# Kernel tuning notes

Hardware: AMD Instinct MI355X
Metric: run time of the kernel (lower is better)

Reference implementation:

```python
import jax, jax.numpy as jnp
import numpy as np

N = 200          # fixed by map_norm's .view(200, 1)
D = 8192         # in_features
EPS = 1e-5


def setup_inputs() -> dict:
    key = jax.random.key(0)
    ks = jax.random.split(key, 7)
    lim = float(np.sqrt(6.0 / D))
    x = jax.random.normal(ks[0], (N, D), dtype=jnp.float32)
    Wq = jax.random.uniform(ks[1], (D, D), dtype=jnp.float32, minval=-lim, maxval=lim)
    Wk = jax.random.uniform(ks[2], (D, D), dtype=jnp.float32, minval=-lim, maxval=lim)
    Wv = jax.random.uniform(ks[3], (D, D), dtype=jnp.float32, minval=-lim, maxval=lim)
    bq = jax.random.normal(ks[4], (D,), dtype=jnp.float32) * 0.01
    bk = jax.random.normal(ks[5], (D,), dtype=jnp.float32) * 0.01
    bv = jax.random.normal(ks[6], (D,), dtype=jnp.float32) * 0.01
    return {"x": x, "Wq": Wq, "bq": bq, "Wk": Wk, "bk": bk, "Wv": Wv, "bv": bv}


def reference(x, Wq, bq, Wk, bk, Wv, bv):
    d_out = x.shape[1]
    cc = jnp.sqrt(jnp.asarray(d_out, dtype=x.dtype))
    # nn.Linear: y = x @ W.T + b
    q = x @ Wq.T + bq          # [N, D]
    k = x @ Wk.T + bk          # [N, D]
    v = x @ Wv.T + bv          # [N, D]
    s = q @ k.T                # [N, N] score map
    mean = jnp.mean(s, axis=-1, keepdims=True)
    var = jnp.var(s, axis=-1, keepdims=True, ddof=1)  # torch.var is unbiased
    s = (s - mean) / jnp.sqrt(var + EPS)
    s = jnp.sin(s)
    scores = jax.nn.softmax(s / cc, axis=-1)
    return scores @ v          # [N, D]
```

## Files before the change

### kernel.cpp

```cpp
#include <hip/hip_runtime.h>
#include <hip/hip_bf16.h>
#include <cstdint>

#define DD 8192
#define NROW 200
#define MT 13
#define MPAD 208
#define KPV 256
#define EPSV 1e-5f
#define BK 64
#define ABUF_BYTES (MPAD * BK * 2)

using short8 = __attribute__((ext_vector_type(8))) short;
using f32x4  = __attribute__((ext_vector_type(4))) float;

#define MEMBAR asm volatile("" ::: "memory")

__device__ __forceinline__ ushort f2bf(float f) {
    union { float f; unsigned u; } c; c.f = f;
    unsigned u = c.u;
    return (ushort)((u + 0x7FFFu + ((u >> 16) & 1u)) >> 16);
}

__device__ __forceinline__ short8 pack8(float4 a, float4 b) {
    short8 o;
    o[0]=f2bf(a.x); o[1]=f2bf(a.y); o[2]=f2bf(a.z); o[3]=f2bf(a.w);
    o[4]=f2bf(b.x); o[5]=f2bf(b.y); o[6]=f2bf(b.z); o[7]=f2bf(b.w);
    return o;
}

__global__ void cvt_x(const float* __restrict__ x, ushort* __restrict__ xb) {
    int i = (blockIdx.x * 256 + threadIdx.x) * 8;
    int row = i >> 13;
    int col = i & (DD - 1);
    short8 o;
    if (row < NROW) {
        const float4* p = reinterpret_cast<const float4*>(x + (size_t)row * DD + col);
        float4 a = p[0], b = p[1];
        o = pack8(a, b);
    } else {
        for (int j = 0; j < 8; ++j) o[j] = 0;
    }
    *reinterpret_cast<short8*>(xb + i) = o;
}

__global__ __launch_bounds__(64) void qkv_gemm(
    const ushort* __restrict__ xb,
    const float* __restrict__ Wq, const float* __restrict__ Wk, const float* __restrict__ Wv,
    const float* __restrict__ bq, const float* __restrict__ bk, const float* __restrict__ bv,
    ushort* __restrict__ qb, ushort* __restrict__ kb, ushort* __restrict__ vt)
{
    __shared__ char Asm[2 * ABUF_BYTES];

    const int mat = blockIdx.y;
    const float* W    = (mat == 0) ? Wq : (mat == 1 ? Wk : Wv);
    const float* bias = (mat == 0) ? bq : (mat == 1 ? bk : bv);

    const int lane  = threadIdx.x;
    const int col16 = lane & 15;
    const int kgrp  = lane >> 4;
    const int ncol0 = blockIdx.x * 32 + col16;
    const int ncol1 = ncol0 + 16;

    const float* wp0 = W + (size_t)ncol0 * DD + kgrp * 8;
    const float* wp1 = W + (size_t)ncol1 * DD + kgrp * 8;

    const ushort* sbase = xb + (size_t)(lane >> 3) * DD
                             + (size_t)(((lane & 7) ^ ((lane >> 3) & 7)) * 8);

    const int b0off = col16 * 128 + ((kgrp ^ (col16 & 7)) * 16);
    const int b1off = b0off ^ 64;

    f32x4 acc0[MT], acc1[MT];
    #pragma unroll
    for (int m = 0; m < MT; ++m)
        for (int r = 0; r < 4; ++r) { acc0[m][r] = 0.f; acc1[m][r] = 0.f; }

#define STAGE(B, KK) { _Pragma("unroll") for (int r = 0; r < 26; ++r) { \
        __builtin_amdgcn_global_load_lds( \
            (const __attribute__((address_space(1))) void*)(sbase + (KK) + r * 8 * DD), \
            (__attribute__((address_space(3))) void*)(Asm + (B) * ABUF_BYTES + r * 1024), \
            16, 0, 0); } }

#define LOADW(d, KK) { \
        d##0 = *reinterpret_cast<const float4*>(wp0 + (KK)); \
        d##1 = *reinterpret_cast<const float4*>(wp0 + (KK) + 4); \
        d##2 = *reinterpret_cast<const float4*>(wp0 + (KK) + 32); \
        d##3 = *reinterpret_cast<const float4*>(wp0 + (KK) + 36); \
        d##4 = *reinterpret_cast<const float4*>(wp1 + (KK)); \
        d##5 = *reinterpret_cast<const float4*>(wp1 + (KK) + 4); \
        d##6 = *reinterpret_cast<const float4*>(wp1 + (KK) + 32); \
        d##7 = *reinterpret_cast<const float4*>(wp1 + (KK) + 36); }

#define COMPUTE(BASE, b00, b01, b10, b11) { \
        _Pragma("unroll") for (int m = 0; m < MT; ++m) { \
            short8 a0 = *reinterpret_cast<const short8*>(Asm + (BASE) + b0off + m * 2048); \
            acc0[m] = __builtin_amdgcn_mfma_f32_16x16x32_bf16(a0, b00, acc0[m], 0, 0, 0); \
            acc1[m] = __builtin_amdgcn_mfma_f32_16x16x32_bf16(a0, b10, acc1[m], 0, 0, 0); \
            short8 a1 = *reinterpret_cast<const short8*>(Asm + (BASE) + b1off + m * 2048); \
            acc0[m] = __builtin_amdgcn_mfma_f32_16x16x32_bf16(a1, b01, acc0[m], 0, 0, 0); \
            acc1[m] = __builtin_amdgcn_mfma_f32_16x16x32_bf16(a1, b11, acc1[m], 0, 0, 0); } }

    float4 wA0, wA1, wA2, wA3, wA4, wA5, wA6, wA7;
    float4 wB0, wB1, wB2, wB3, wB4, wB5, wB6, wB7;

    STAGE(0, 0);
    MEMBAR;
    LOADW(wA, 0);
    MEMBAR;
    LOADW(wB, BK);
    MEMBAR;

    for (int k0 = 0; k0 < DD; k0 += 2 * BK) {
        {
            short8 b00 = pack8(wA0, wA1);
            short8 b01 = pack8(wA2, wA3);
            short8 b10 = pack8(wA4, wA5);
            short8 b11 = pack8(wA6, wA7);
            STAGE(1, k0 + BK);
            MEMBAR;
            int kp = (k0 + 2 * BK) & (DD - 1);
            LOADW(wA, kp);
            MEMBAR;
            asm volatile("s_waitcnt vmcnt(42)" ::: "memory");
            COMPUTE(0, b00, b01, b10, b11);
        }
        {
            short8 b00 = pack8(wB0, wB1);
            short8 b01 = pack8(wB2, wB3);
            short8 b10 = pack8(wB4, wB5);
            short8 b11 = pack8(wB6, wB7);
            int kp1 = (k0 + 2 * BK) & (DD - 1);
            STAGE(0, kp1);
            MEMBAR;
            int kp2 = (k0 + 3 * BK) & (DD - 1);
            LOADW(wB, kp2);
            MEMBAR;
            asm volatile("s_waitcnt vmcnt(42)" ::: "memory");
            COMPUTE(ABUF_BYTES, b00, b01, b10, b11);
        }
    }
#undef STAGE
#undef LOADW
#undef COMPUTE

    const float badd0 = bias[ncol0];
    const float badd1 = bias[ncol1];
    if (mat < 2) {
        ushort* outb = (mat == 0) ? qb : kb;
        #pragma unroll
        for (int m = 0; m < MT; ++m)
            for (int r = 0; r < 4; ++r) {
                int row = m * 16 + kgrp * 4 + r;
                outb[(size_t)row * DD + ncol0] = f2bf(acc0[m][r] + badd0);
                outb[(size_t)row * DD + ncol1] = f2bf(acc1[m][r] + badd1);
            }
    } else {
        #pragma unroll
        for (int m = 0; m < MT; ++m)
            for (int r = 0; r < 4; ++r) {
                int row = m * 16 + kgrp * 4 + r;
                vt[(size_t)ncol0 * KPV + row] = f2bf(acc0[m][r] + badd0);
                vt[(size_t)ncol1 * KPV + row] = f2bf(acc1[m][r] + badd1);
            }
    }
}

__global__ __launch_bounds__(256) void sgemm(const ushort* __restrict__ qb, const ushort* __restrict__ kb,
                                             float* __restrict__ sbuf) {
    const int bm = blockIdx.y, bn = blockIdx.x;
    const int lane  = threadIdx.x & 63;
    const int wave  = threadIdx.x >> 6;
    const int col16 = lane & 15, kgrp = lane >> 4;
    const ushort* ap = qb + (size_t)(bm * 16 + col16) * DD + kgrp * 8;
    const ushort* bp = kb + (size_t)(bn * 16 + col16) * DD + kgrp * 8;
    f32x4 acc;
    for (int r = 0; r < 4; ++r) acc[r] = 0.f;
    const int kend = (wave + 1) * 2048;
    for (int k0 = wave * 2048; k0 < kend; k0 += 32) {
        short8 a = *reinterpret_cast<const short8*>(ap + k0);
        short8 b = *reinterpret_cast<const short8*>(bp + k0);
        acc = __builtin_amdgcn_mfma_f32_16x16x32_bf16(a, b, acc, 0, 0, 0);
    }
    __shared__ f32x4 red[4][64];
    red[wave][lane] = acc;
    __syncthreads();
    if (wave == 0) {
        f32x4 s = red[0][lane];
        for (int j = 1; j < 4; ++j) { f32x4 o = red[j][lane]; for (int r = 0; r < 4; ++r) s[r] += o[r]; }
        for (int r = 0; r < 4; ++r)
            sbuf[(size_t)(bm * 16 + kgrp * 4 + r) * MPAD + bn * 16 + col16] = s[r];
    }
}

__global__ __launch_bounds__(256) void rownorm(const float* __restrict__ sbuf, ushort* __restrict__ pb) {
    const int row = blockIdx.x;
    const int t = threadIdx.x;
    if (row >= NROW) { pb[(size_t)row * KPV + t] = 0; return; }
    __shared__ float part[4];
    const int lane = t & 63, wave = t >> 6;
    float x = (t < NROW) ? sbuf[(size_t)row * MPAD + t] : 0.f;

    float s = x;
    for (int m = 32; m; m >>= 1) s += __shfl_xor(s, m, 64);
    if (lane == 0) part[wave] = s;
    __syncthreads();
    float mean = (part[0] + part[1] + part[2] + part[3]) * (1.f / 200.f);

    float d = (t < NROW) ? (x - mean) : 0.f;
    float s2 = d * d;
    for (int m = 32; m; m >>= 1) s2 += __shfl_xor(s2, m, 64);
    __syncthreads();
    if (lane == 0) part[wave] = s2;
    __syncthreads();
    float var = (part[0] + part[1] + part[2] + part[3]) * (1.f / 199.f);

    float inv = 1.f / sqrtf(var + EPSV);
    float y = sinf(d * inv);
    const float inv_cc = 1.f / 90.50966799187809f;
    float e = (t < NROW) ? expf(y * inv_cc) : 0.f;

    float se = e;
    for (int m = 32; m; m >>= 1) se += __shfl_xor(se, m, 64);
    __syncthreads();
    if (lane == 0) part[wave] = se;
    __syncthreads();
    float tot = part[0] + part[1] + part[2] + part[3];
    pb[(size_t)row * KPV + t] = (t < NROW) ? f2bf(e / tot) : (ushort)0;
}

__global__ __launch_bounds__(256) void pv_gemm(const ushort* __restrict__ pb, const ushort* __restrict__ vt,
                                               float* __restrict__ out) {
    const int lane  = threadIdx.x & 63;
    const int wave  = threadIdx.x >> 6;
    const int col16 = lane & 15, kgrp = lane >> 4;
    const int ncol  = blockIdx.x * 64 + wave * 16 + col16;
    const ushort* ap = pb + (size_t)col16 * KPV + kgrp * 8;
    const ushort* bp = vt + (size_t)ncol  * KPV + kgrp * 8;
    f32x4 acc[MT];
    for (int m = 0; m < MT; ++m)
        for (int r = 0; r < 4; ++r) acc[m][r] = 0.f;
    for (int k0 = 0; k0 < KPV; k0 += 32) {
        short8 b = *reinterpret_cast<const short8*>(bp + k0);
        #pragma unroll
        for (int m = 0; m < MT; ++m) {
            short8 a = *reinterpret_cast<const short8*>(ap + (size_t)m * 16 * KPV + k0);
            acc[m] = __builtin_amdgcn_mfma_f32_16x16x32_bf16(a, b, acc[m], 0, 0, 0);
        }
    }
    for (int m = 0; m < MT; ++m)
        for (int r = 0; r < 4; ++r) {
            int row = m * 16 + kgrp * 4 + r;
            if (row < NROW) out[(size_t)row * DD + ncol] = acc[m][r];
        }
}

extern "C" void kernel_launch(void* const* d_in, const int* in_sizes, int n_in,
                              void* d_out, int out_size, void* d_ws, size_t ws_size,
                              hipStream_t stream) {
    const float* x  = (const float*)d_in[0];
    const float* Wq = (const float*)d_in[1];
    const float* bq = (const float*)d_in[2];
    const float* Wk = (const float*)d_in[3];
    const float* bk = (const float*)d_in[4];
    const float* Wv = (const float*)d_in[5];
    const float* bv = (const float*)d_in[6];
    float* out = (float*)d_out;

    char* ws = (char*)d_ws;
    ushort* xb   = (ushort*)(ws);
    ushort* qb   = (ushort*)(ws + 3407872);
    ushort* kb   = (ushort*)(ws + 6815744);
    ushort* vt   = (ushort*)(ws + 10223616);
    float*  sbuf = (float*)(ws + 14417920);
    ushort* pb   = (ushort*)(ws + 14590976);

    cvt_x<<<832, 256, 0, stream>>>(x, xb);
    qkv_gemm<<<dim3(256, 3), 64, 0, stream>>>(xb, Wq, Wk, Wv, bq, bk, bv, qb, kb, vt);
    sgemm<<<dim3(13, 13), 256, 0, stream>>>(qb, kb, sbuf);
    rownorm<<<208, 256, 0, stream>>>(sbuf, pb);
    pv_gemm<<<128, 256, 0, stream>>>(pb, vt, out);
}
```

Before: 284.2 us.

## Split QKV GEMM over K with 4-wave blocks sharing staged X tile

The QKV projection kernel now runs 256-thread blocks in which four waves share one LDS-staged X tile, each wave loading part of it. Blocks synchronise with barriers and the pipeline is a single double-buffered phase loop. When the workspace is large enough, K is split four ways. fp32 partial sums go to a workspace buffer and two new kernels reduce them, add the bias, convert to bf16 and transpose V. This aims to raise the number of waves per CU and improve latency hiding for the weight-bandwidth-bound GEMM, at the cost of extra partial-sum traffic, two extra launches and barrier overhead.

```diff
diff --git a/kernel.cpp b/kernel.cpp
--- a/kernel.cpp
+++ b/kernel.cpp
@@ -44,11 +44,12 @@
     *reinterpret_cast<short8*>(xb + i) = o;
 }
 
-__global__ __launch_bounds__(64) void qkv_gemm(
+__global__ __launch_bounds__(256, 3) void qkv_gemm(
     const ushort* __restrict__ xb,
     const float* __restrict__ Wq, const float* __restrict__ Wk, const float* __restrict__ Wv,
     const float* __restrict__ bq, const float* __restrict__ bk, const float* __restrict__ bv,
-    ushort* __restrict__ qb, ushort* __restrict__ kb, ushort* __restrict__ vt)
+    ushort* __restrict__ qb, ushort* __restrict__ kb, ushort* __restrict__ vt,
+    float* __restrict__ part, int kchunk)
 {
     __shared__ char Asm[2 * ABUF_BYTES];
 
@@ -56,17 +57,23 @@
     const float* W    = (mat == 0) ? Wq : (mat == 1 ? Wk : Wv);
     const float* bias = (mat == 0) ? bq : (mat == 1 ? bk : bv);
 
-    const int lane  = threadIdx.x;
+    const int t     = threadIdx.x;
+    const int lane  = t & 63;
+    const int wave  = t >> 6;
     const int col16 = lane & 15;
     const int kgrp  = lane >> 4;
-    const int ncol0 = blockIdx.x * 32 + col16;
+    const int ncol0 = blockIdx.x * 128 + wave * 32 + col16;
     const int ncol1 = ncol0 + 16;
+    const int kbase = blockIdx.z * kchunk;
+    const int kmask = kchunk - 1;
 
     const float* wp0 = W + (size_t)ncol0 * DD + kgrp * 8;
     const float* wp1 = W + (size_t)ncol1 * DD + kgrp * 8;
 
     const ushort* sbase = xb + (size_t)(lane >> 3) * DD
                              + (size_t)(((lane & 7) ^ ((lane >> 3) & 7)) * 8);
+    const int r0w = (wave < 2) ? wave * 7 : 14 + (wave - 2) * 6;
+    const int sw  = (wave < 2) ? 7 : 6;
 
     const int b0off = col16 * 128 + ((kgrp ^ (col16 & 7)) * 16);
     const int b1off = b0off ^ 64;
@@ -76,11 +83,11 @@
     for (int m = 0; m < MT; ++m)
         for (int r = 0; r < 4; ++r) { acc0[m][r] = 0.f; acc1[m][r] = 0.f; }
 
-#define STAGE(B, KK) { _Pragma("unroll") for (int r = 0; r < 26; ++r) { \
+#define STAGE(BOFF, KK) { _Pragma("unroll") for (int rr = 0; rr < 7; ++rr) { if (rr < sw) { \
         __builtin_amdgcn_global_load_lds( \
-            (const __attribute__((address_space(1))) void*)(sbase + (KK) + r * 8 * DD), \
-            (__attribute__((address_space(3))) void*)(Asm + (B) * ABUF_BYTES + r * 1024), \
-            16, 0, 0); } }
+            (const __attribute__((address_space(1))) void*)(sbase + (KK) + (size_t)(r0w + rr) * 8 * DD), \
+            (__attribute__((address_space(3))) void*)(Asm + (BOFF) + (r0w + rr) * 1024), \
+            16, 0, 0); } } }
 
 #define LOADW(d, KK) { \
         d##0 = *reinterpret_cast<const float4*>(wp0 + (KK)); \
@@ -101,69 +108,121 @@
             acc0[m] = __builtin_amdgcn_mfma_f32_16x16x32_bf16(a1, b01, acc0[m], 0, 0, 0); \
             acc1[m] = __builtin_amdgcn_mfma_f32_16x16x32_bf16(a1, b11, acc1[m], 0, 0, 0); } }
 
-    float4 wA0, wA1, wA2, wA3, wA4, wA5, wA6, wA7;
-    float4 wB0, wB1, wB2, wB3, wB4, wB5, wB6, wB7;
-
-    STAGE(0, 0);
+    float4 w0, w1, w2, w3, w4, w5, w6, w7;
+
+    LOADW(w, kbase);
     MEMBAR;
-    LOADW(wA, 0);
+    STAGE(0, kbase);
     MEMBAR;
-    LOADW(wB, BK);
-    MEMBAR;
-
-    for (int k0 = 0; k0 < DD; k0 += 2 * BK) {
-        {
-            short8 b00 = pack8(wA0, wA1);
-            short8 b01 = pack8(wA2, wA3);
-            short8 b10 = pack8(wA4, wA5);
-            short8 b11 = pack8(wA6, wA7);
-            STAGE(1, k0 + BK);
-            MEMBAR;
-            int kp = (k0 + 2 * BK) & (DD - 1);
-            LOADW(wA, kp);
-            MEMBAR;
-            asm volatile("s_waitcnt vmcnt(42)" ::: "memory");
-            COMPUTE(0, b00, b01, b10, b11);
-        }
-        {
-            short8 b00 = pack8(wB0, wB1);
-            short8 b01 = pack8(wB2, wB3);
-            short8 b10 = pack8(wB4, wB5);
-            short8 b11 = pack8(wB6, wB7);
-            int kp1 = (k0 + 2 * BK) & (DD - 1);
-            STAGE(0, kp1);
-            MEMBAR;
-            int kp2 = (k0 + 3 * BK) & (DD - 1);
-            LOADW(wB, kp2);
-            MEMBAR;
-            asm volatile("s_waitcnt vmcnt(42)" ::: "memory");
-            COMPUTE(ABUF_BYTES, b00, b01, b10, b11);
-        }
+
+    const int nph = kchunk / BK;
+    int k0 = 0;
+    for (int ph = 0; ph < nph; ++ph) {
+        short8 b00 = pack8(w0, w1);
+        short8 b01 = pack8(w2, w3);
+        short8 b10 = pack8(w4, w5);
+        short8 b11 = pack8(w6, w7);
+        MEMBAR;
+        int knext = kbase + ((k0 + BK) & kmask);
+        LOADW(w, knext);
+        MEMBAR;
+        STAGE(((ph + 1) & 1) * ABUF_BYTES, knext);
+        MEMBAR;
+        if (sw == 7) asm volatile("s_waitcnt vmcnt(15)" ::: "memory");
+        else         asm volatile("s_waitcnt vmcnt(14)" ::: "memory");
+        asm volatile("s_barrier" ::: "memory");
+        COMPUTE((ph & 1) * ABUF_BYTES, b00, b01, b10, b11);
+        asm volatile("s_barrier" ::: "memory");
+        k0 += BK;
     }
 #undef STAGE
 #undef LOADW
 #undef COMPUTE
 
-    const float badd0 = bias[ncol0];
-    const float badd1 = bias[ncol1];
-    if (mat < 2) {
-        ushort* outb = (mat == 0) ? qb : kb;
+    if (gridDim.z == 1) {
+        const float badd0 = bias[ncol0];
+        const float badd1 = bias[ncol1];
+        if (mat < 2) {
+            ushort* outb = (mat == 0) ? qb : kb;
+            #pragma unroll
+            for (int m = 0; m < MT; ++m)
+                for (int r = 0; r < 4; ++r) {
+                    int row = m * 16 + kgrp * 4 + r;
+                    outb[(size_t)row * DD + ncol0] = f2bf(acc0[m][r] + badd0);
+                    outb[(size_t)row * DD + ncol1] = f2bf(acc1[m][r] + badd1);
+                }
+        } else {
+            #pragma unroll
+            for (int m = 0; m < MT; ++m)
+                for (int r = 0; r < 4; ++r) {
+                    int row = m * 16 + kgrp * 4 + r;
+                    vt[(size_t)ncol0 * KPV + row] = f2bf(acc0[m][r] + badd0);
+                    vt[(size_t)ncol1 * KPV + row] = f2bf(acc1[m][r] + badd1);
+                }
+        }
+    } else {
+        float* pp = part + ((size_t)mat * gridDim.z + blockIdx.z) * ((size_t)MPAD * DD);
         #pragma unroll
         for (int m = 0; m < MT; ++m)
             for (int r = 0; r < 4; ++r) {
                 int row = m * 16 + kgrp * 4 + r;
-                outb[(size_t)row * DD + ncol0] = f2bf(acc0[m][r] + badd0);
-                outb[(size_t)row * DD + ncol1] = f2bf(acc1[m][r] + badd1);
+                pp[(size_t)row * DD + ncol0] = acc0[m][r];
+                pp[(size_t)row * DD + ncol1] = acc1[m][r];
             }
-    } else {
-        #pragma unroll
-        for (int m = 0; m < MT; ++m)
-            for (int r = 0; r < 4; ++r) {
-                int row = m * 16 + kgrp * 4 + r;
-                vt[(size_t)ncol0 * KPV + row] = f2bf(acc0[m][r] + badd0);
-                vt[(size_t)ncol1 * KPV + row] = f2bf(acc1[m][r] + badd1);
-            }
-    }
+    }
+}
+
+__global__ __launch_bounds__(256) void cvt_qk(const float* __restrict__ part,
+                                              const float* __restrict__ bq, const float* __restrict__ bk,
+                                              ushort* __restrict__ qb, ushort* __restrict__ kb, int ks) {
+    const int mat = blockIdx.z;
+    const int row = blockIdx.y;
+    const int col = blockIdx.x * 2048 + threadIdx.x * 8;
+    const float* bias = mat ? bk : bq;
+    float s[8];
+    {
+        const float4 b0 = *reinterpret_cast<const float4*>(bias + col);
+        const float4 b1 = *reinterpret_cast<const float4*>(bias + col + 4);
+        s[0]=b0.x; s[1]=b0.y; s[2]=b0.z; s[3]=b0.w; s[4]=b1.x; s[5]=b1.y; s[6]=b1.z; s[7]=b1.w;
+    }
+    const float* pm = part + (size_t)mat * ks * MPAD * DD + (size_t)row * DD + col;
+    for (int p = 0; p < ks; ++p) {
+        const float4 a0 = *reinterpret_cast<const float4*>(pm + (size_t)p * MPAD * DD);
+        const float4 a1 = *reinterpret_cast<const float4*>(pm + (size_t)p * MPAD * DD + 4);
+        s[0]+=a0.x; s[1]+=a0.y; s[2]+=a0.z; s[3]+=a0.w; s[4]+=a1.x; s[5]+=a1.y; s[6]+=a1.z; s[7]+=a1.w;
+    }
+    short8 o;
+    for (int j = 0; j < 8; ++j) o[j] = f2bf(s[j]);
+    ushort* outb = mat ? kb : qb;
+    *reinterpret_cast<short8*>(outb + (size_t)row * DD + col) = o;
+}
+
+__global__ void vtrans_r(const float* __restrict__ pv, const float* __restrict__ bv,
+                         ushort* __restrict__ vt, int ks) {
+    __shared__ float lds[64][65];
+    const int t  = threadIdx.x;
+    const int n0 = blockIdx.x * 64;
+    const int k0 = blockIdx.y * 64;
+    #pragma unroll
+    for (int r = 0; r < 16; ++r) {
+        int kl = r * 4 + (t >> 6);
+        int nl = t & 63;
+        int k  = k0 + kl;
+        float v = 0.f;
+        if (k < NROW) {
+            v = bv[n0 + nl];
+            for (int p = 0; p < ks; ++p)
+                v += pv[(size_t)p * MPAD * DD + (size_t)k * DD + n0 + nl];
+        }
+        lds[nl][kl] = v;
+    }
+    __syncthreads();
+    int nl   = t >> 2;
+    int koff = (t & 3) * 16;
+    short8 o0, o1;
+    for (int j = 0; j < 8; ++j) { o0[j] = f2bf(lds[nl][koff + j]); o1[j] = f2bf(lds[nl][koff + 8 + j]); }
+    short8* dst = reinterpret_cast<short8*>(vt + (size_t)(n0 + nl) * KPV + k0 + koff);
+    dst[0] = o0; dst[1] = o1;
 }
 
 __global__ __launch_bounds__(256) void sgemm(const ushort* __restrict__ qb, const ushort* __restrict__ kb,
@@ -274,9 +333,21 @@
     ushort* vt   = (ushort*)(ws + 10223616);
     float*  sbuf = (float*)(ws + 14417920);
     ushort* pb   = (ushort*)(ws + 14590976);
+    float*  part = (float*)(ws + 14697472);
+
+    const size_t need4 = 14697472u + (size_t)3 * 4 * MPAD * DD * 4;
+    const int ks = (ws_size >= need4) ? 4 : 1;
 
     cvt_x<<<832, 256, 0, stream>>>(x, xb);
-    qkv_gemm<<<dim3(256, 3), 64, 0, stream>>>(xb, Wq, Wk, Wv, bq, bk, bv, qb, kb, vt);
+    if (ks == 4) {
+        qkv_gemm<<<dim3(64, 3, 4), 256, 0, stream>>>(xb, Wq, Wk, Wv, bq, bk, bv,
+                                                     qb, kb, vt, part, DD / 4);
+        cvt_qk<<<dim3(4, MPAD, 2), 256, 0, stream>>>(part, bq, bk, qb, kb, 4);
+        vtrans_r<<<dim3(128, 4), 256, 0, stream>>>(part + (size_t)2 * 4 * MPAD * DD, bv, vt, 4);
+    } else {
+        qkv_gemm<<<dim3(64, 3, 1), 256, 0, stream>>>(xb, Wq, Wk, Wv, bq, bk, bv,
+                                                     qb, kb, vt, part, DD);
+    }
     sgemm<<<dim3(13, 13), 256, 0, stream>>>(qb, kb, sbuf);
     rownorm<<<208, 256, 0, stream>>>(sbuf, pb);
     pv_gemm<<<128, 256, 0, stream>>>(pb, vt, out);
```

New measurement: 422.1 us. 48.5% more time.
